# Kernel tuning notes

Hardware: AMD Instinct MI355X
Metric: run time of the kernel (lower is better)

## Reference

```python
import jax, jax.numpy as jnp
import numpy as np

N_NODES = 50000
N_UND = 200000  # undirected edges; total directed E = 2*N_UND
D = 128
EPS = 1e-10


def setup_inputs() -> dict:
    key = jax.random.key(0)
    ks = jax.random.split(key, 10)
    x = jax.random.normal(ks[0], (N_NODES, D), dtype=jnp.float32)
    W1 = jax.random.normal(ks[1], (D, D), dtype=jnp.float32) / np.sqrt(D)
    W2 = jax.random.normal(ks[2], (D, D), dtype=jnp.float32) / np.sqrt(D)
    We1 = jax.random.normal(ks[3], (2 * D, D), dtype=jnp.float32) / np.sqrt(2 * D)
    we2 = jax.random.normal(ks[4], (D,), dtype=jnp.float32) / np.sqrt(D)
    Wc1 = jax.random.normal(ks[5], (D, D), dtype=jnp.float32) / np.sqrt(D)
    Wc2 = jax.random.normal(ks[6], (D, D), dtype=jnp.float32) / np.sqrt(D)
    # undirected edge list: each edge stored in both directions so the
    # transpose/reorder_like symmetrization is a known static permutation
    s = jax.random.randint(ks[7], (N_UND,), 0, N_NODES)
    d = jax.random.randint(ks[8], (N_UND,), 0, N_NODES)
    src = jnp.concatenate([s, d])
    dst = jnp.concatenate([d, s])
    edge_index = jnp.stack([src, dst]).astype(jnp.int64)  # [2, 2*N_UND]
    noise_u = jax.random.uniform(ks[9], (2 * N_UND,), dtype=jnp.float32,
                                 minval=EPS, maxval=1.0 - EPS)
    return {"x": x, "W1": W1, "W2": W2, "We1": We1, "we2": we2,
            "Wc1": Wc1, "Wc2": Wc2, "noise_u": noise_u,
            "edge_index": edge_index}


def reference(x, W1, W2, We1, we2, Wc1, Wc2, noise_u, edge_index):
    N = x.shape[0]
    src, dst = edge_index[0], edge_index[1]

    # --- clf.get_emb: one message-passing layer ---
    h = x @ W1                                              # [N, D]
    agg = jax.ops.segment_sum(h[src], dst, num_segments=N)  # scatter-add
    emb = jax.nn.relu(x @ W2 + agg)                         # [N, D]

    # --- extractor: edge attention logits from gathered endpoint embs ---
    e_feat = jnp.concatenate([emb[src], emb[dst]], axis=-1)  # [E, 2D]
    att_log_logits = jnp.tanh(e_feat @ We1) @ we2            # [E]

    # --- Gumbel-sigmoid sampling (training=True, temp=1) ---
    noise = jnp.log(noise_u) - jnp.log1p(-noise_u)
    att = jax.nn.sigmoid(att_log_logits + noise)             # [E]

    # --- undirected symmetrization: (att + att_reversed_edge) / 2 ---
    half = att.shape[0] // 2
    att_rev = jnp.concatenate([att[half:], att[:half]])
    edge_att = (att + att_rev) * 0.5                         # [E]

    # --- clf forward with edge_atten: attention-weighted scatter-add ---
    hc = x @ Wc1                                             # [N, D]
    aggc = jax.ops.segment_sum(edge_att[:, None] * hc[src], dst,
                               num_segments=N)               # [N, D]
    x_out = jax.nn.relu(x @ Wc2 + aggc)                      # xwhole [N, D]
    return x_out
```

## Files before the change

kernel.cpp:

```cpp
#include <hip/hip_runtime.h>
#include <math.h>

#define N_NODES 50000
#define N_EDGES 400000
#define E_HALF  200000
#define D 128

template <int NG, int RELU_IN>
__global__ __launch_bounds__(256) void gemm_multi(
    const float* __restrict__ x,
    const float* __restrict__ W0, const float* __restrict__ W1,
    const float* __restrict__ W2, const float* __restrict__ W3,
    float* __restrict__ O0, float* __restrict__ O1,
    float* __restrict__ O2, float* __restrict__ O3)
{
    __shared__ float ws[16][128];
    __shared__ float xt[128][132];

    const float* Wg[4] = {W0, W1, W2, W3};
    float*       Og[4] = {O0, O1, O2, O3};

    const int tid  = threadIdx.x;
    const int row0 = blockIdx.x * 128;

    for (int i = tid * 4; i < 128 * D; i += 256 * 4) {
        const int row = i >> 7;
        const int col = i & 127;
        const int r   = row0 + row;
        float4 v;
        if (r < N_NODES) {
            v = *(const float4*)&x[(size_t)r * D + col];
        } else {
            v = make_float4(0.f, 0.f, 0.f, 0.f);
        }
        if (RELU_IN) {
            v.x = fmaxf(v.x, 0.f); v.y = fmaxf(v.y, 0.f);
            v.z = fmaxf(v.z, 0.f); v.w = fmaxf(v.w, 0.f);
        }
        xt[col + 0][row] = v.x;
        xt[col + 1][row] = v.y;
        xt[col + 2][row] = v.z;
        xt[col + 3][row] = v.w;
    }

    const int ty  = tid >> 4;
    const int tx  = tid & 15;
    const int r0  = ty * 8;
    const int c0a = tx * 4;
    const int c0b = 64 + tx * 4;

    #pragma unroll
    for (int g = 0; g < NG; ++g) {
        const float* W = Wg[g];

        float acc[8][8];
        #pragma unroll
        for (int r = 0; r < 8; ++r)
            #pragma unroll
            for (int c = 0; c < 8; ++c) acc[r][c] = 0.f;

        for (int kc = 0; kc < 8; ++kc) {
            __syncthreads();
            for (int i = tid * 4; i < 16 * D; i += 256 * 4) {
                *(float4*)&ws[0][0 + i] = *(const float4*)&W[kc * 16 * D + i];
            }
            __syncthreads();

            const int kbase = kc * 16;
            #pragma unroll 4
            for (int k2 = 0; k2 < 16; ++k2) {
                const float4 wa = *(const float4*)&ws[k2][c0a];
                const float4 wb = *(const float4*)&ws[k2][c0b];
                const float4 x0 = *(const float4*)&xt[kbase + k2][r0];
                const float4 x1 = *(const float4*)&xt[kbase + k2][r0 + 4];
                const float wv[8] = {wa.x, wa.y, wa.z, wa.w,
                                     wb.x, wb.y, wb.z, wb.w};
                const float xr[8] = {x0.x, x0.y, x0.z, x0.w,
                                     x1.x, x1.y, x1.z, x1.w};
                #pragma unroll
                for (int r = 0; r < 8; ++r) {
                    #pragma unroll
                    for (int c = 0; c < 8; ++c)
                        acc[r][c] = fmaf(xr[r], wv[c], acc[r][c]);
                }
            }
        }

        float* O = Og[g];
        #pragma unroll
        for (int r = 0; r < 8; ++r) {
            const int row = row0 + r0 + r;
            if (row < N_NODES) {
                float4 oa = make_float4(acc[r][0], acc[r][1], acc[r][2], acc[r][3]);
                float4 ob = make_float4(acc[r][4], acc[r][5], acc[r][6], acc[r][7]);
                *(float4*)&O[(size_t)row * D + c0a] = oa;
                *(float4*)&O[(size_t)row * D + c0b] = ob;
            }
        }
    }
}

__global__ __launch_bounds__(256) void zero_kernel(int* __restrict__ p, int n)
{
    const int i = blockIdx.x * 256 + threadIdx.x;
    if (i < n) p[i] = 0;
}

__global__ __launch_bounds__(256) void hist_kernel(
    const int* __restrict__ dst, int* __restrict__ cnt)
{
    const int e = blockIdx.x * 256 + threadIdx.x;
    if (e < N_EDGES) atomicAdd(&cnt[dst[e]], 1);
}

#define SCAN_NB 196

__global__ __launch_bounds__(256) void scan_partial(
    const int* __restrict__ cnt, int* __restrict__ exc, int* __restrict__ bsum)
{
    __shared__ int sh[256];
    const int t   = threadIdx.x;
    const int idx = blockIdx.x * 256 + t;
    const int v   = (idx < N_NODES) ? cnt[idx] : 0;
    sh[t] = v;
    __syncthreads();
    #pragma unroll
    for (int d = 1; d < 256; d <<= 1) {
        const int tv = (t >= d) ? sh[t - d] : 0;
        __syncthreads();
        sh[t] += tv;
        __syncthreads();
    }
    if (idx < N_NODES) exc[idx] = sh[t] - v;
    if (t == 255) bsum[blockIdx.x] = sh[255];
}

__global__ __launch_bounds__(256) void scan_block(
    const int* __restrict__ bsum, int* __restrict__ bscan)
{
    __shared__ int sh[256];
    const int t = threadIdx.x;
    const int v = (t < SCAN_NB) ? bsum[t] : 0;
    sh[t] = v;
    __syncthreads();
    #pragma unroll
    for (int d = 1; d < 256; d <<= 1) {
        const int tv = (t >= d) ? sh[t - d] : 0;
        __syncthreads();
        sh[t] += tv;
        __syncthreads();
    }
    if (t < SCAN_NB) bscan[t] = sh[t] - v;
}

__global__ __launch_bounds__(256) void scan_final(
    const int* __restrict__ exc, const int* __restrict__ bscan,
    int* __restrict__ off, int* __restrict__ cursor)
{
    const int idx = blockIdx.x * 256 + threadIdx.x;
    if (idx < N_NODES) {
        const int o = exc[idx] + bscan[blockIdx.x];
        off[idx]    = o;
        cursor[idx] = o;
    }
    if (idx == 0) off[N_NODES] = N_EDGES;
}

__global__ __launch_bounds__(256) void bucket_kernel(
    const int* __restrict__ src, const int* __restrict__ dst,
    int* __restrict__ cursor, int* __restrict__ csr_src, int* __restrict__ csr_eid)
{
    const int e = blockIdx.x * 256 + threadIdx.x;
    if (e >= N_EDGES) return;
    const int pos = atomicAdd(&cursor[dst[e]], 1);
    csr_src[pos] = src[e];
    csr_eid[pos] = e;
}

__global__ __launch_bounds__(256) void gather_sum(
    const int* __restrict__ off, const int* __restrict__ csr_src,
    const float* __restrict__ h, float* __restrict__ emb)
{
    const int t    = blockIdx.x * 256 + threadIdx.x;
    const int node = t >> 6;
    const int lane = t & 63;
    if (node >= N_NODES) return;
    const int beg = off[node];
    const int end = off[node + 1];
    const size_t o = (size_t)node * D + lane * 2;
    float2 acc = *(const float2*)&emb[o];
    for (int j = beg; j < end; ++j) {
        const int s = csr_src[j];
        const float2 v = *(const float2*)&h[(size_t)s * D + lane * 2];
        acc.x += v.x; acc.y += v.y;
    }
    *(float2*)&emb[o] = acc;
}

__global__ __launch_bounds__(256) void gather_watt_relu(
    const int* __restrict__ off, const int* __restrict__ csr_src,
    const int* __restrict__ csr_eid, const float* __restrict__ att,
    const float* __restrict__ hc, float* __restrict__ out)
{
    const int t    = blockIdx.x * 256 + threadIdx.x;
    const int node = t >> 6;
    const int lane = t & 63;
    if (node >= N_NODES) return;
    const int beg = off[node];
    const int end = off[node + 1];
    const size_t o = (size_t)node * D + lane * 2;
    float2 acc = *(const float2*)&out[o];
    for (int j = beg; j < end; ++j) {
        const int s   = csr_src[j];
        const int eid = csr_eid[j];
        const int pr  = (eid < E_HALF) ? (eid + E_HALF) : (eid - E_HALF);
        const float w = 0.5f * (att[eid] + att[pr]);
        const float2 v = *(const float2*)&hc[(size_t)s * D + lane * 2];
        acc.x = fmaf(w, v.x, acc.x);
        acc.y = fmaf(w, v.y, acc.y);
    }
    acc.x = fmaxf(acc.x, 0.f);
    acc.y = fmaxf(acc.y, 0.f);
    *(float2*)&out[o] = acc;
}

__device__ __forceinline__ float fast_tanh(float v)
{
    const float e = __expf(2.f * v);
    return 1.f - 2.f / (e + 1.f);
}

__global__ __launch_bounds__(256) void edge_logits(
    const int* __restrict__ src, const int* __restrict__ dst,
    const float* __restrict__ A, const float* __restrict__ B,
    const float* __restrict__ we2, const float* __restrict__ noise_u,
    float* __restrict__ att)
{
    const int t    = blockIdx.x * 256 + threadIdx.x;
    const int e    = t >> 5;
    const int lane = t & 31;
    if (e >= N_EDGES) return;
    const int s = src[e];
    const int d = dst[e];
    const float4 a = *(const float4*)&A[(size_t)s * D + lane * 4];
    const float4 b = *(const float4*)&B[(size_t)d * D + lane * 4];
    const float4 w = *(const float4*)&we2[lane * 4];
    float p = fast_tanh(a.x + b.x) * w.x + fast_tanh(a.y + b.y) * w.y +
              fast_tanh(a.z + b.z) * w.z + fast_tanh(a.w + b.w) * w.w;
    #pragma unroll
    for (int off = 16; off >= 1; off >>= 1)
        p += __shfl_xor(p, off, 32);
    if (lane == 0) {
        const float u = noise_u[e];
        const float z = p + logf(u) - log1pf(-u);
        att[e] = 1.f / (1.f + __expf(-z));
    }
}

extern "C" void kernel_launch(void* const* d_in, const int* in_sizes, int n_in,
                              void* d_out, int out_size, void* d_ws, size_t ws_size,
                              hipStream_t stream)
{
    const float* x      = (const float*)d_in[0];
    const float* W1     = (const float*)d_in[1];
    const float* W2     = (const float*)d_in[2];
    const float* We1    = (const float*)d_in[3];
    const float* we2    = (const float*)d_in[4];
    const float* Wc1    = (const float*)d_in[5];
    const float* Wc2    = (const float*)d_in[6];
    const float* noiseu = (const float*)d_in[7];
    const int*   eidx   = (const int*)d_in[8];

    const int* src = eidx;
    const int* dst = eidx + N_EDGES;

    float* out = (float*)d_out;

    float* wsf = (float*)d_ws;
    float* h   = wsf;
    float* hc  = wsf +  6400000;
    float* emb = wsf + 12800000;
    float* att = wsf + 19200000;
    int* ibase   = (int*)(wsf + 19600000);
    int* cnt     = ibase;
    int* off     = ibase + 50000;
    int* cursor  = ibase + 100001;
    int* exc     = ibase + 150001;
    int* bsum    = ibase + 200001;
    int* bscan   = ibase + 200257;
    int* csr_src = ibase + 262144;
    int* csr_eid = csr_src + N_EDGES;

    const int row_tiles = (N_NODES + 127) / 128;
    const int edge_blk  = (N_EDGES + 255) / 256;
    const int node_blk  = (N_NODES * 64 + 255) / 256;
    const int elog_blk  = (N_EDGES * 32 + 255) / 256;

    zero_kernel<<<(N_NODES + 255) / 256, 256, 0, stream>>>(cnt, N_NODES);
    hist_kernel<<<edge_blk, 256, 0, stream>>>(dst, cnt);
    scan_partial<<<SCAN_NB, 256, 0, stream>>>(cnt, exc, bsum);
    scan_block<<<1, 256, 0, stream>>>(bsum, bscan);
    scan_final<<<SCAN_NB, 256, 0, stream>>>(exc, bscan, off, cursor);
    bucket_kernel<<<edge_blk, 256, 0, stream>>>(src, dst, cursor, csr_src, csr_eid);

    gemm_multi<4, 0><<<row_tiles, 256, 0, stream>>>(
        x, W1, W2, Wc1, Wc2, h, emb, hc, out);

    gather_sum<<<node_blk, 256, 0, stream>>>(off, csr_src, h, emb);

    gemm_multi<2, 1><<<row_tiles, 256, 0, stream>>>(
        emb, We1, We1 + D * D, nullptr, nullptr, h, emb, nullptr, nullptr);

    edge_logits<<<elog_blk, 256, 0, stream>>>(src, dst, h, emb, we2, noiseu, att);

    gather_watt_relu<<<node_blk, 256, 0, stream>>>(off, csr_src, csr_eid, att, hc, out);
}
```

Measured before the change: 479.3 us.

## Compute weight-matrix pairs together with double-buffered weight tiles in GEMM

Restructures the multi-output GEMM to process two weight matrices per pass, so each shared-memory x value read feeds two accumulator sets. Weight tiles are now 4 rows, loaded from global memory in a double-buffered ping-pong that overlaps the next tile's load with compute. Holding 128 accumulators per thread greatly raises register pressure and may spill or lower occupancy. The code also assumes an even number of outputs.

Result: slower. 507.0 us (+5.8%).

```diff
diff --git a/kernel.cpp b/kernel.cpp
--- a/kernel.cpp
+++ b/kernel.cpp
@@ -14,7 +14,7 @@
     float* __restrict__ O0, float* __restrict__ O1,
     float* __restrict__ O2, float* __restrict__ O3)
 {
-    __shared__ float ws[16][128];
+    __shared__ float ws[2][2][4][128];
     __shared__ float xt[128][132];
 
     const float* Wg[4] = {W0, W1, W2, W3};
@@ -49,52 +49,107 @@
     const int c0a = tx * 4;
     const int c0b = 64 + tx * 4;
 
+    const int sm = tid >> 7;
+    const int si = (tid & 127) * 4;
+    const int sr = si >> 7;
+    const int sc = si & 127;
+
     #pragma unroll
-    for (int g = 0; g < NG; ++g) {
-        const float* W = Wg[g];
-
-        float acc[8][8];
+    for (int gp = 0; gp < NG / 2; ++gp) {
+        const float* WA = Wg[2 * gp];
+        const float* WB = Wg[2 * gp + 1];
+        const float* Wp = (sm == 0) ? WA : WB;
+
+        float accA[8][8], accB[8][8];
         #pragma unroll
         for (int r = 0; r < 8; ++r)
             #pragma unroll
-            for (int c = 0; c < 8; ++c) acc[r][c] = 0.f;
-
-        for (int kc = 0; kc < 8; ++kc) {
+            for (int c = 0; c < 8; ++c) { accA[r][c] = 0.f; accB[r][c] = 0.f; }
+
+        *(float4*)&ws[0][sm][sr][sc] = *(const float4*)&Wp[(size_t)sr * D + sc];
+        __syncthreads();
+
+        #pragma unroll 1
+        for (int kc = 0; kc < 32; kc += 2) {
+            if (kc + 1 < 32) {
+                *(float4*)&ws[1][sm][sr][sc] =
+                    *(const float4*)&Wp[(size_t)(kc + 1) * 4 * D + sr * D + sc];
+            }
+            {
+                const int kbase = kc * 4;
+                #pragma unroll
+                for (int k2 = 0; k2 < 4; ++k2) {
+                    const float4 wa0 = *(const float4*)&ws[0][0][k2][c0a];
+                    const float4 wb0 = *(const float4*)&ws[0][0][k2][c0b];
+                    const float4 wa1 = *(const float4*)&ws[0][1][k2][c0a];
+                    const float4 wb1 = *(const float4*)&ws[0][1][k2][c0b];
+                    const float4 x0  = *(const float4*)&xt[kbase + k2][r0];
+                    const float4 x1  = *(const float4*)&xt[kbase + k2][r0 + 4];
+                    const float wv0[8] = {wa0.x, wa0.y, wa0.z, wa0.w,
+                                          wb0.x, wb0.y, wb0.z, wb0.w};
+                    const float wv1[8] = {wa1.x, wa1.y, wa1.z, wa1.w,
+                                          wb1.x, wb1.y, wb1.z, wb1.w};
+                    const float xr[8]  = {x0.x, x0.y, x0.z, x0.w,
+                                          x1.x, x1.y, x1.z, x1.w};
+                    #pragma unroll
+                    for (int r = 0; r < 8; ++r) {
+                        #pragma unroll
+                        for (int c = 0; c < 8; ++c) {
+                            accA[r][c] = fmaf(xr[r], wv0[c], accA[r][c]);
+                            accB[r][c] = fmaf(xr[r], wv1[c], accB[r][c]);
+                        }
+                    }
+                }
+            }
             __syncthreads();
-            for (int i = tid * 4; i < 16 * D; i += 256 * 4) {
-                *(float4*)&ws[0][0 + i] = *(const float4*)&W[kc * 16 * D + i];
+
+            if (kc + 2 < 32) {
+                *(float4*)&ws[0][sm][sr][sc] =
+                    *(const float4*)&Wp[(size_t)(kc + 2) * 4 * D + sr * D + sc];
+            }
+            {
+                const int kbase = (kc + 1) * 4;
+                #pragma unroll
+                for (int k2 = 0; k2 < 4; ++k2) {
+                    const float4 wa0 = *(const float4*)&ws[1][0][k2][c0a];
+                    const float4 wb0 = *(const float4*)&ws[1][0][k2][c0b];
+                    const float4 wa1 = *(const float4*)&ws[1][1][k2][c0a];
+                    const float4 wb1 = *(const float4*)&ws[1][1][k2][c0b];
+                    const float4 x0  = *(const float4*)&xt[kbase + k2][r0];
+                    const float4 x1  = *(const float4*)&xt[kbase + k2][r0 + 4];
+                    const float wv0[8] = {wa0.x, wa0.y, wa0.z, wa0.w,
+                                          wb0.x, wb0.y, wb0.z, wb0.w};
+                    const float wv1[8] = {wa1.x, wa1.y, wa1.z, wa1.w,
+                                          wb1.x, wb1.y, wb1.z, wb1.w};
+                    const float xr[8]  = {x0.x, x0.y, x0.z, x0.w,
+                                          x1.x, x1.y, x1.z, x1.w};
+                    #pragma unroll
+                    for (int r = 0; r < 8; ++r) {
+                        #pragma unroll
+                        for (int c = 0; c < 8; ++c) {
+                            accA[r][c] = fmaf(xr[r], wv0[c], accA[r][c]);
+                            accB[r][c] = fmaf(xr[r], wv1[c], accB[r][c]);
+                        }
+                    }
+                }
             }
             __syncthreads();
-
-            const int kbase = kc * 16;
-            #pragma unroll 4
-            for (int k2 = 0; k2 < 16; ++k2) {
-                const float4 wa = *(const float4*)&ws[k2][c0a];
-                const float4 wb = *(const float4*)&ws[k2][c0b];
-                const float4 x0 = *(const float4*)&xt[kbase + k2][r0];
-                const float4 x1 = *(const float4*)&xt[kbase + k2][r0 + 4];
-                const float wv[8] = {wa.x, wa.y, wa.z, wa.w,
-                                     wb.x, wb.y, wb.z, wb.w};
-                const float xr[8] = {x0.x, x0.y, x0.z, x0.w,
-                                     x1.x, x1.y, x1.z, x1.w};
-                #pragma unroll
-                for (int r = 0; r < 8; ++r) {
-                    #pragma unroll
-                    for (int c = 0; c < 8; ++c)
-                        acc[r][c] = fmaf(xr[r], wv[c], acc[r][c]);
-                }
-            }
         }
 
-        float* O = Og[g];
+        float* OA = Og[2 * gp];
+        float* OB = Og[2 * gp + 1];
         #pragma unroll
         for (int r = 0; r < 8; ++r) {
             const int row = row0 + r0 + r;
             if (row < N_NODES) {
-                float4 oa = make_float4(acc[r][0], acc[r][1], acc[r][2], acc[r][3]);
-                float4 ob = make_float4(acc[r][4], acc[r][5], acc[r][6], acc[r][7]);
-                *(float4*)&O[(size_t)row * D + c0a] = oa;
-                *(float4*)&O[(size_t)row * D + c0b] = ob;
+                *(float4*)&OA[(size_t)row * D + c0a] =
+                    make_float4(accA[r][0], accA[r][1], accA[r][2], accA[r][3]);
+                *(float4*)&OA[(size_t)row * D + c0b] =
+                    make_float4(accA[r][4], accA[r][5], accA[r][6], accA[r][7]);
+                *(float4*)&OB[(size_t)row * D + c0a] =
+                    make_float4(accB[r][0], accB[r][1], accB[r][2], accB[r][3]);
+                *(float4*)&OB[(size_t)row * D + c0b] =
+                    make_float4(accB[r][4], accB[r][5], accB[r][6], accB[r][7]);
             }
         }
     }
```
